# Kernel optimization log

Hardware: AMD Instinct MI355X
Metric: run time of the kernel (lower is better)

Reference implementation:

```python
import jax, jax.numpy as jnp
import numpy as np

SEQ_LEN = 4096
D_MODEL = 1024
OUT_DIM = 1024
KERNEL = 256
STRIDE = 16
NUM_HEADS = 16


def _p(key, *shape):
    return jax.random.normal(key, shape, dtype=jnp.float32) * 0.02


def setup_inputs() -> dict:
    key = jax.random.key(0)
    ks = jax.random.split(key, 12)
    return {
        "path": jax.random.normal(ks[0], (SEQ_LEN, D_MODEL), dtype=jnp.float32),
        # sliding_module (nn.MultiheadAttention, embed_dim=D_MODEL)
        "w_in1": _p(ks[1], 3 * D_MODEL, D_MODEL),
        "b_in1": jnp.zeros((3 * D_MODEL,), jnp.float32),
        "w_out1": _p(ks[2], D_MODEL, D_MODEL),
        "b_out1": jnp.zeros((D_MODEL,), jnp.float32),
        # linear_module
        "w_lin": _p(ks[3], OUT_DIM, D_MODEL),
        "b_lin": jnp.zeros((OUT_DIM,), jnp.float32),
        # accum_module (embed_dim=OUT_DIM)
        "w_in2": _p(ks[4], 3 * OUT_DIM, OUT_DIM),
        "b_in2": jnp.zeros((3 * OUT_DIM,), jnp.float32),
        "w_out2": _p(ks[5], OUT_DIM, OUT_DIM),
        "b_out2": jnp.zeros((OUT_DIM,), jnp.float32),
    }


def _mha(q, k, v, w_in, b_in, w_out, b_out, num_heads):
    """torch nn.MultiheadAttention math (dropout=0). q,k,v: [..., L, E]."""
    E = q.shape[-1]
    Dh = E // num_heads
    wq, wk, wv = jnp.split(w_in, 3, axis=0)
    bq, bk, bv = jnp.split(b_in, 3)
    def heads(t):
        return t.reshape(t.shape[:-1] + (num_heads, Dh))
    qh = heads(q @ wq.T + bq)
    kh = heads(k @ wk.T + bk)
    vh = heads(v @ wv.T + bv)
    scale = 1.0 / np.sqrt(Dh).astype(np.float32)
    att = jax.nn.softmax(jnp.einsum("...qhd,...khd->...hqk", qh, kh) * scale, axis=-1)
    out = jnp.einsum("...hqk,...khd->...qhd", att, vh)
    out = out.reshape(out.shape[:-2] + (E,))
    return out @ w_out.T + b_out


def reference(path, w_in1, b_in1, w_out1, b_out1, w_lin, b_lin,
              w_in2, b_in2, w_out2, b_out2):
    seq_len = path.shape[-2]
    slices_num = (seq_len - KERNEL) // STRIDE
    # overlapping windows: [slices_num, KERNEL, D_MODEL]
    idx = jnp.arange(slices_num)[:, None] * STRIDE + jnp.arange(KERNEL)[None, :]
    x = path[idx]
    # batched self-attention over windows
    x = _mha(x, x, x, w_in1, b_in1, w_out1, b_out1, NUM_HEADS)
    x = jax.nn.relu(x @ w_lin.T + b_lin)  # [slices_num, KERNEL, OUT_DIM]
    # sequential recurrent attention accumulation
    def step(cum_att, xi):
        new = _mha(xi, cum_att, cum_att, w_in2, b_in2, w_out2, b_out2, NUM_HEADS)
        return new, None
    cum_att, _ = jax.lax.scan(step, x[0], x[1:])
    return cum_att  # [KERNEL, OUT_DIM]
```

## Files before the change

kernel.cpp:

```cpp
#include <hip/hip_runtime.h>
#include <math.h>

#define D_MODEL 1024
#define N_WIN   240
#define TOK     256
#define NH      16
#define DH      64
#define CHUNK   8
#define NCHUNK  30
#define WIN     ((size_t)TOK * D_MODEL)

typedef unsigned short ushort_t;
typedef unsigned long long ull_t;
typedef __attribute__((ext_vector_type(8))) short short8;
typedef __attribute__((ext_vector_type(4))) float floatx4;

__device__ __forceinline__ ushort_t f2bf(float f) {
    unsigned u = __float_as_uint(f);
    unsigned lsb = (u >> 16) & 1u;
    u += 0x7fffu + lsb;
    return (ushort_t)(u >> 16);
}

__device__ __forceinline__ void st2_wt(ushort_t* p, ushort_t v) {
    unsigned vv = v;
    asm volatile("global_store_short %0, %1, off sc1"
                 :: "v"(p), "v"(vv) : "memory");
}
__device__ __forceinline__ void rel_drain() {
    asm volatile("s_waitcnt vmcnt(0)" ::: "memory");
}

#define GLDS(g, l) __builtin_amdgcn_global_load_lds( \
    (const __attribute__((address_space(1))) unsigned int*)(g), \
    (__attribute__((address_space(3))) unsigned int*)(l), 16, 0, 0)

__device__ __forceinline__ void grid_bar(unsigned* base, int g, unsigned s)
{
    rel_drain();
    __syncthreads();
    if (threadIdx.x == 0) {
        unsigned old = __hip_atomic_fetch_add(base + g * 32, 1u,
                __ATOMIC_RELAXED, __HIP_MEMORY_SCOPE_AGENT);
        if (old == 8u * s - 1u) {
            unsigned r = __hip_atomic_fetch_add(base + 256, 1u,
                    __ATOMIC_RELAXED, __HIP_MEMORY_SCOPE_AGENT);
            if (r == 8u * s - 1u)
                __hip_atomic_store(base + 288, s, __ATOMIC_RELAXED,
                                   __HIP_MEMORY_SCOPE_AGENT);
        }
        while (__hip_atomic_load(base + 288, __ATOMIC_RELAXED,
                                 __HIP_MEMORY_SCOPE_AGENT) < s)
            __builtin_amdgcn_s_sleep(1);
    }
    __syncthreads();
}

__device__ __forceinline__ void help_bar(unsigned* base, int g, unsigned s)
{
    rel_drain();
    __syncthreads();
    if (threadIdx.x == 0) {
        unsigned old = __hip_atomic_fetch_add(base + 1024 + g * 32, 1u,
                __ATOMIC_RELAXED, __HIP_MEMORY_SCOPE_AGENT);
        if (old == 8u * s - 1u) {
            unsigned r = __hip_atomic_fetch_add(base + 1800, 1u,
                    __ATOMIC_RELAXED, __HIP_MEMORY_SCOPE_AGENT);
            if (r == 24u * s - 1u)
                __hip_atomic_store(base + 1832, s, __ATOMIC_RELAXED,
                                   __HIP_MEMORY_SCOPE_AGENT);
        }
        while (__hip_atomic_load(base + 1832, __ATOMIC_RELAXED,
                                 __HIP_MEMORY_SCOPE_AGENT) < s)
            __builtin_amdgcn_s_sleep(1);
    }
    __syncthreads();
}

__global__ __launch_bounds__(256) void cast_bf_k(
    const float* __restrict__ s, ushort_t* __restrict__ d, int n)
{
    int i = (blockIdx.x * 256 + threadIdx.x) * 4;
    if (i >= n) return;
    float4 v = *(const float4*)(s + i);
    ushort4 o;
    o.x = f2bf(v.x); o.y = f2bf(v.y); o.z = f2bf(v.z); o.w = f2bf(v.w);
    *(ushort4*)(d + i) = o;
}

// ... 3 lines not shown
    __shared__ ushort_t t[64][65];
    const int bx = blockIdx.x * 64, by = blockIdx.y * 64;
    const int c = threadIdx.x & 63, r0 = threadIdx.x >> 6;
#pragma unroll
    for (int k = 0; k < 16; ++k) {
        int r = r0 + k * 4;
        t[r][c] = src[(size_t)(by + r) * 1024 + bx + c];
    }
    __syncthreads();
#pragma unroll
    for (int k = 0; k < 16; ++k) {
        int r = r0 + k * 4;
        dst[(size_t)(bx + r) * 1024 + by + c] = t[c][r];
    }
}

__global__ __launch_bounds__(256) void bc_k(
    const float* __restrict__ w_in2, const float* __restrict__ b_in2,
    const float* __restrict__ b_out2, float* __restrict__ bc)
{
    int n = blockIdx.x * 256 + threadIdx.x;
    const float* row = w_in2 + (size_t)(1024 + n) * 1024;
    float s = b_in2[1024 + n];
    for (int j = 0; j < 1024; j += 4) {
        float4 w = *(const float4*)(row + j);
        float4 b = *(const float4*)(b_out2 + j);
        s += w.x * b.x + w.y * b.y + w.z * b.z + w.w * b.w;
    }
    bc[n] = s;
}

template<bool GATHER, bool WT>
__device__ __forceinline__ void gemm_core(
    ushort_t* As, ushort_t* Bs,
    const ushort_t* __restrict__ A, int lda, int w0,
    const ushort_t* __restrict__ W, const float* __restrict__ bias,
    ushort_t* __restrict__ Cb, float* __restrict__ Cf, int ldc,
    int K, int m0, int n0, int co, int relu)
{
    const int tid = threadIdx.x;
    const int wave = tid >> 6, lane = tid & 63;
    const int wm = wave & 1, wn = wave >> 1;

    int r0 = m0 + (tid >> 2), r1 = r0 + 64;
    if (GATHER) {
        r0 = (w0 + (r0 >> 8)) * 16 + (r0 & 255);
        r1 = (w0 + (r1 >> 8)) * 16 + (r1 & 255);
    }
    const int kcol = (tid & 3) * 8;
    const ushort_t* gA0 = A + (size_t)r0 * lda + kcol;
    const ushort_t* gA1 = A + (size_t)r1 * lda + kcol;
    const ushort_t* pW  = W + (size_t)n0 * K;
    const ushort_t* gB0 = pW + (size_t)(tid >> 2) * K + kcol;
    const ushort_t* gB1 = gB0 + (size_t)64 * K;
    ushort_t* lA = As + wave * 512;
    ushort_t* lB = Bs + wave * 512;

    floatx4 acc[4][4];
#pragma unroll
    for (int i = 0; i < 4; ++i)
#pragma unroll
        for (int j = 0; j < 4; ++j) acc[i][j] = (floatx4){0.f, 0.f, 0.f, 0.f};

    const int fr = lane & 15, fk = (lane >> 4) * 8;
    const int arow = (wm * 64 + fr) * 32 + fk;
    const int brow = (wn * 64 + fr) * 32 + fk;

    for (int k0 = 0; k0 < K; k0 += 32) {
        GLDS(gA0 + k0, lA);
        GLDS(gA1 + k0, lA + 2048);
        GLDS(gB0 + k0, lB);
        GLDS(gB1 + k0, lB + 2048);
        __syncthreads();
// ... 13 lines not shown

    const int crq = (lane >> 4) * 4;
    const int ccol = lane & 15;
#pragma unroll
    for (int mi = 0; mi < 4; ++mi) {
#pragma unroll
        for (int ni = 0; ni < 4; ++ni) {
            int lc = wn * 64 + ni * 16 + ccol;
            float bz = bias[n0 + lc];
#pragma unroll
            for (int rg = 0; rg < 4; ++rg) {
                int row = m0 + wm * 64 + mi * 16 + crq + rg;
                float v = acc[mi][ni][rg] + bz;
                if (relu) v = fmaxf(v, 0.f);
                size_t off = (size_t)row * ldc + co + lc;
                if (Cb) {
                    if (WT) st2_wt(Cb + off, f2bf(v));
                    else    Cb[off] = f2bf(v);
                }
                if (Cf) Cf[off] = v;
            }
        }
    }
}

__global__ __launch_bounds__(256) void gemm_bf_k(
    const ushort_t* __restrict__ A, int lda,
    const ushort_t* __restrict__ W, const float* __restrict__ bias,
    ushort_t* __restrict__ Cb, float* __restrict__ Cf, int ldc,
    int K, int relu)
{
    __shared__ ushort_t As[128 * 32];
    __shared__ ushort_t Bs[128 * 32];
    gemm_core<false, false>(As, Bs, A, lda, 0, W, bias, Cb, Cf, ldc, K,
                            blockIdx.y * 128, blockIdx.x * 128, blockIdx.x * 128, relu);
}

__global__ __launch_bounds__(256) void gemm_qkv_k(
    const ushort_t* __restrict__ path_bf, const ushort_t* __restrict__ W,
    const float* __restrict__ bias, ushort_t* __restrict__ Cb, int w0)
{
    __shared__ ushort_t As[128 * 32];
    __shared__ ushort_t Bs[128 * 32];
    gemm_core<true, false>(As, Bs, path_bf, 1024, w0, W, bias, Cb, nullptr, 3072, 1024,
                           blockIdx.y * 128, blockIdx.x * 128, blockIdx.x * 128, 0);
}

#define PLD 260
#define VLD 132

struct AttnShared {
    ushort_t P[64 * PLD];
    ushort_t VT[64 * VLD];
    float    l[64];
};

__device__ void attn_body(AttnShared& sh,
    const ushort_t* __restrict__ qkv, ushort_t* __restrict__ ao,
    int rs, int h, int b)
{
    const ushort_t* base = qkv + (size_t)b * TOK * 3072;
    const ushort_t* Q = base;
    const ushort_t* K = base + 1024;
    const ushort_t* V = base + 2048;
    ushort_t* O = ao + (size_t)b * TOK * 1024;
    const int ldq = 3072, ldkv = 3072, ldo = 1024;
    const int tid = threadIdx.x;
    const int wave = tid >> 6, lane = tid & 63;
    const int fr = lane & 15, q = lane >> 4, fk = q * 8;
    const ushort_t* Qh = Q + (size_t)(rs * 64) * ldq + h * 64;
    const ushort_t* Kh = K + h * 64;
    const ushort_t* Vh = V + h * 64;
    const int m0 = wave * 16;

    floatx4 s[16];
#pragma unroll
    for (int nt = 0; nt < 16; ++nt) s[nt] = (floatx4){0.f, 0.f, 0.f, 0.f};
#pragma unroll
    for (int kc = 0; kc < 64; kc += 32) {
        short8 a = *(const short8*)(Qh + (size_t)(m0 + fr) * ldq + kc + fk);
#pragma unroll
        for (int nt = 0; nt < 16; ++nt) {
            short8 b2 = *(const short8*)(Kh + (size_t)(nt * 16 + fr) * ldkv + kc + fk);
            s[nt] = __builtin_amdgcn_mfma_f32_16x16x32_bf16(a, b2, s[nt], 0, 0, 0);
        }
    }

    float rmax[4] = {-INFINITY, -INFINITY, -INFINITY, -INFINITY};
#pragma unroll
    for (int nt = 0; nt < 16; ++nt)
#pragma unroll
        for (int rg = 0; rg < 4; ++rg) rmax[rg] = fmaxf(rmax[rg], s[nt][rg]);
#pragma unroll
    for (int d = 1; d < 16; d <<= 1)
#pragma unroll
        for (int rg = 0; rg < 4; ++rg)
            rmax[rg] = fmaxf(rmax[rg], __shfl_xor(rmax[rg], d));

    float rsum[4] = {0.f, 0.f, 0.f, 0.f};
#pragma unroll
// ... 39 lines not shown
            }
        }
        __syncthreads();
#pragma unroll
        for (int ks = 0; ks < 4; ++ks) {
            short8 a = *(const short8*)&sh.P[(m0 + fr) * PLD + half * 128 + ks * 32 + fk];
#pragma unroll
            for (int nt2 = 0; nt2 < 4; ++nt2) {
                short8 b2 = *(const short8*)&sh.VT[(nt2 * 16 + fr) * VLD + ks * 32 + fk];
                o[nt2] = __builtin_amdgcn_mfma_f32_16x16x32_bf16(a, b2, o[nt2], 0, 0, 0);
            }
        }
        __syncthreads();
    }

    float linv[4];
#pragma unroll
    for (int rg = 0; rg < 4; ++rg) linv[rg] = 1.f / sh.l[m0 + q * 4 + rg];
#pragma unroll
    for (int nt2 = 0; nt2 < 4; ++nt2)
#pragma unroll
        for (int rg = 0; rg < 4; ++rg) {
            int row = rs * 64 + m0 + q * 4 + rg;
            st2_wt(O + (size_t)row * ldo + h * 64 + nt2 * 16 + fr,
                   f2bf(o[nt2][rg] * linv[rg]));
        }
    __syncthreads();
}

__global__ __launch_bounds__(256) void attn_mfma_k(
    const ushort_t* __restrict__ qkv, ushort_t* __restrict__ ao)
{
    __shared__ AttnShared sh;
    attn_body(sh, qkv, ao, blockIdx.x, blockIdx.y, blockIdx.z);
}

#define KLD 72
#define TLD 264

struct ScanSmem {
    union {
        struct { ushort_t Ab[2][16384]; ushort_t Wb[2][8192]; } st;
        struct { ushort_t Kl[256 * KLD]; ushort_t Vt[64 * TLD];
                 ushort_t P[64 * TLD]; } at;
    };
};

__device__ __forceinline__ void stage_kv(
    const ushort_t* __restrict__ Asrc, const ushort_t* __restrict__ Wsel,
    int h, int k0, ushort_t* __restrict__ Ad, ushort_t* __restrict__ Wd,
    int wave, int lane)
{
#pragma unroll
    for (int t = 0; t < 8; ++t) {
        int j = wave * 512 + t * 64 + lane;
        int row = j >> 3;
        int blk = (j & 7) ^ (row & 7);
        GLDS(Asrc + (size_t)row * 1024 + k0 + blk * 8,
             Ad + wave * 4096 + t * 512);
    }
#pragma unroll
    for (int t = 0; t < 4; ++t) {
        int j = wave * 256 + t * 64 + lane;
        int r = j >> 3;
        int blk = (j & 7) ^ (r & 7);
        int n = ((r >> 6) << 10) + h * 64 + (r & 63);
        GLDS(Wsel + (size_t)n * 1024 + k0 + blk * 8,
             Wd + wave * 2048 + t * 512);
    }
}

__device__ void scan_body(
    ScanSmem& sm, int h, int rs, int g,
    const ushort_t* __restrict__ Qchunk, int i0, int w0, int nsteps,
    const ushort_t* __restrict__ x0, ushort_t* __restrict__ AOb,
    const ushort_t* __restrict__ Wkv, const float* __restrict__ bkv,
    const ushort_t* __restrict__ Wc, const float* __restrict__ bc,
    unsigned* __restrict__ bar, unsigned s0)
{
    const int tid = threadIdx.x;
    const int wave = tid >> 6, lane = tid & 63;
    const int fr = lane & 15, q = lane >> 4, fk = q * 8;

    float bkK[4], bkV[4], bcK[4], bcV[4];
#pragma unroll
    for (int nt = 0; nt < 4; ++nt) {
        bkK[nt] = bkv[h * 64 + nt * 16 + fr];
        bkV[nt] = bkv[1024 + h * 64 + nt * 16 + fr];
        bcK[nt] = bc[h * 64 + nt * 16 + fr];
        bcV[nt] = bc[1024 + h * 64 + nt * 16 + fr];
    }

    ushort_t* Kl = sm.at.Kl;
    ushort_t* Vt = sm.at.Vt;
    ushort_t* P  = sm.at.P;

    unsigned s = s0;
    for (int t0 = 0; t0 < nsteps; ++t0, ++s) {
        const int i = i0 + t0;
        const ushort_t* Asrc;
        const ushort_t* Wsel;
        if (i == 1) { Asrc = x0; Wsel = Wkv; }
        else {
            Asrc = AOb + (size_t)((i - 1) & 7) * WIN;
            Wsel = Wc;
        }

        const int m0g = rs * 64 + wave * 16;
        const ushort_t* Qrow = Qchunk + (size_t)(i - w0) * WIN
            + (size_t)(m0g + fr) * 1024 + h * 64;
        short8 qf0 = *(const short8*)(Qrow);
        short8 qf1 = *(const short8*)(Qrow + 32);

        floatx4 acc[4][8];
#pragma unroll
        for (int mt = 0; mt < 4; ++mt)
#pragma unroll
            for (int nt = 0; nt < 8; ++nt)
                acc[mt][nt] = (floatx4){0.f, 0.f, 0.f, 0.f};

        stage_kv(Asrc, Wsel, h, 0, sm.st.Ab[0], sm.st.Wb[0], wave, lane);
#pragma unroll 1
        for (int t = 0; t < 16; ++t) {
            const int cur = t & 1;
            if (t < 15) {
                stage_kv(Asrc, Wsel, h, (t + 1) * 64,
                         sm.st.Ab[cur ^ 1], sm.st.Wb[cur ^ 1], wave, lane);
                asm volatile("s_waitcnt vmcnt(12)" ::: "memory");
            } else {
                asm volatile("s_waitcnt vmcnt(0)" ::: "memory");
            }
            __builtin_amdgcn_s_barrier();
            const ushort_t* Ac = sm.st.Ab[cur];
            const ushort_t* Wc_ = sm.st.Wb[cur];
#pragma unroll
            for (int kh = 0; kh < 2; ++kh) {
                const int pb = (((kh << 2) + q) ^ (fr & 7)) * 8;
                short8 a[4];
#pragma unroll
                for (int mt = 0; mt < 4; ++mt)
                    a[mt] = *(const short8*)
                        &Ac[(wave * 64 + mt * 16 + fr) * 64 + pb];
#pragma unroll
                for (int nt = 0; nt < 8; ++nt) {
                    const int r = ((nt >> 2) << 6) + ((nt & 3) << 4) + fr;
                    short8 b = *(const short8*)&Wc_[r * 64 + pb];
#pragma unroll
                    for (int mt = 0; mt < 4; ++mt)
                        acc[mt][nt] = __builtin_amdgcn_mfma_f32_16x16x32_bf16(
                            a[mt], b, acc[mt][nt], 0, 0, 0);
                }
            }
            asm volatile("s_waitcnt lgkmcnt(0)" ::: "memory");
            __builtin_amdgcn_sched_barrier(0);
            __builtin_amdgcn_s_barrier();
        }

#pragma unroll
        for (int mt = 0; mt < 4; ++mt) {
            const int kb = wave * 64 + mt * 16;
#pragma unroll
            for (int nt = 0; nt < 4; ++nt) {
                float bzk = (i == 1) ? bkK[nt] : bcK[nt];
                float bzv = (i == 1) ? bkV[nt] : bcV[nt];
#pragma unroll
                for (int rg = 0; rg < 4; ++rg)
                    Kl[(kb + q * 4 + rg) * KLD + nt * 16 + fr] =
                        f2bf(acc[mt][nt][rg] + bzk);
                ushort4 pv;
                pv.x = f2bf(acc[mt][nt + 4][0] + bzv);
                pv.y = f2bf(acc[mt][nt + 4][1] + bzv);
                pv.z = f2bf(acc[mt][nt + 4][2] + bzv);
                pv.w = f2bf(acc[mt][nt + 4][3] + bzv);
                *(ushort4*)&Vt[(nt * 16 + fr) * TLD + kb + q * 4] = pv;
            }
        }
        __syncthreads();

        ushort_t* AOcur = AOb + (size_t)(i & 7) * WIN;
        {
            const int pl0 = wave * 16;
            floatx4 sc[16];
#pragma unroll
            for (int nt = 0; nt < 16; ++nt) sc[nt] = (floatx4){0.f, 0.f, 0.f, 0.f};
#pragma unroll
            for (int kc = 0; kc < 64; kc += 32) {
                short8 a = (kc == 0) ? qf0 : qf1;
#pragma unroll
                for (int nt = 0; nt < 16; ++nt) {
                    short8 b = *(const short8*)&Kl[(nt * 16 + fr) * KLD + kc + fk];
                    sc[nt] = __builtin_amdgcn_mfma_f32_16x16x32_bf16(
                        a, b, sc[nt], 0, 0, 0);
                }
            }
            float rmax[4] = {-INFINITY, -INFINITY, -INFINITY, -INFINITY};
#pragma unroll
            for (int nt = 0; nt < 16; ++nt)
#pragma unroll
                for (int rg = 0; rg < 4; ++rg) rmax[rg] = fmaxf(rmax[rg], sc[nt][rg]);
#pragma unroll
            for (int d = 1; d < 16; d <<= 1)
#pragma unroll
                for (int rg = 0; rg < 4; ++rg)
                    rmax[rg] = fmaxf(rmax[rg], __shfl_xor(rmax[rg], d));
            float rsum[4] = {0.f, 0.f, 0.f, 0.f};
#pragma unroll
            for (int nt = 0; nt < 16; ++nt) {
#pragma unroll
                for (int rg = 0; rg < 4; ++rg) {
                    float p = __expf((sc[nt][rg] - rmax[rg]) * 0.125f);
                    rsum[rg] += p;
                    P[(pl0 + q * 4 + rg) * TLD + nt * 16 + fr] = f2bf(p);
                }
            }
#pragma unroll
            for (int d = 1; d < 16; d <<= 1)
#pragma unroll
                for (int rg = 0; rg < 4; ++rg) rsum[rg] += __shfl_xor(rsum[rg], d);

            floatx4 o[4];
#pragma unroll
            for (int nt = 0; nt < 4; ++nt) o[nt] = (floatx4){0.f, 0.f, 0.f, 0.f};
#pragma unroll
            for (int kt = 0; kt < 8; ++kt) {
                short8 a = *(const short8*)&P[(pl0 + fr) * TLD + kt * 32 + fk];
#pragma unroll
                for (int nt = 0; nt < 4; ++nt) {
                    short8 b = *(const short8*)&Vt[(nt * 16 + fr) * TLD + kt * 32 + fk];
                    o[nt] = __builtin_amdgcn_mfma_f32_16x16x32_bf16(
                        a, b, o[nt], 0, 0, 0);
                }
            }
            float linv[4];
#pragma unroll
            for (int rg = 0; rg < 4; ++rg) linv[rg] = 1.f / rsum[rg];
#pragma unroll
            for (int nt = 0; nt < 4; ++nt)
#pragma unroll
                for (int rg = 0; rg < 4; ++rg) {
                    int row = m0g + q * 4 + rg;
                    st2_wt(AOcur + (size_t)row * 1024 + h * 64 + nt * 16 + fr,
                           f2bf(o[nt][rg] * linv[rg]));
                }
        }
        grid_bar(bar, g, s);
    }
}

struct GemmSmem { ushort_t As[128 * 32]; ushort_t Bs[128 * 32]; };
union FusedSmem { ScanSmem scan; GemmSmem gem; AttnShared att; };

__global__ __launch_bounds__(256, 1) void fused_k(
    const ushort_t* __restrict__ Qchunk, int i0, int w0, int nsteps,
    const ushort_t* __restrict__ x0, ushort_t* __restrict__ AOb,
    const ushort_t* __restrict__ Wkv, const float* __restrict__ bkv,
    const ushort_t* __restrict__ Wc, const float* __restrict__ bc,
    unsigned* __restrict__ bar, unsigned s0,
    int do_help, int w0n,
    const ushort_t* __restrict__ path_bf,
    const ushort_t* __restrict__ w_in1, const float* __restrict__ b_in1,
    ushort_t* __restrict__ qkv, ushort_t* __restrict__ ao,
    ushort_t* __restrict__ ybuf,
    const ushort_t* __restrict__ w_out1, const float* __restrict__ b_out1,
    const ushort_t* __restrict__ w_lin, const float* __restrict__ b_lin,
    ushort_t* __restrict__ Xc,
    const ushort_t* __restrict__ w_in2, const float* __restrict__ b_in2,
    ushort_t* __restrict__ Qnext, unsigned hs0)
{
    __shared__ FusedSmem sm;
    const int wg = blockIdx.x;
    const int x = wg & 7, y = wg >> 3;

    if (x < 2) {
        const int scanIdx = x * 32 + y;
        const int h  = (x << 3) | (y >> 2);
        const int rs = y & 3;
        const int g  = scanIdx & 7;
        scan_body(sm.scan, h, rs, g,
                  Qchunk, i0, w0, nsteps, x0, AOb, Wkv, bkv, Wc, bc, bar, s0);
        return;
    }
    if (!do_help) return;

    const int hw = (x - 2) * 32 + y;
    const int hg = hw >> 3;

    for (int t = hw; t < 384; t += 192) {
        int bx = t % 24, by = t / 24;
        gemm_core<true, true>(sm.gem.As, sm.gem.Bs, path_bf, 1024, w0n,
                              w_in1, b_in1, qkv, nullptr, 3072, 1024,
                              by * 128, bx * 128, bx * 128, 0);
    }
    help_bar(bar, hg, hs0);

    for (int t = hw; t < 512; t += 192) {
        int rs = t & 3, h = (t >> 2) & 15, b = t >> 6;
        attn_body(sm.att, qkv, ao, rs, h, b);
    }
    help_bar(bar, hg, hs0 + 1);

    for (int t = hw; t < 128; t += 192) {
        int bx = t & 7, by = t >> 3;
        gemm_core<false, true>(sm.gem.As, sm.gem.Bs, ao, 1024, 0,
                               w_out1, b_out1, ybuf, nullptr, 1024, 1024,
                               by * 128, bx * 128, bx * 128, 0);
    }
    help_bar(bar, hg, hs0 + 2);

    for (int t = hw; t < 128; t += 192) {
        int bx = t & 7, by = t >> 3;
        gemm_core<false, true>(sm.gem.As, sm.gem.Bs, ybuf, 1024, 0,
                               w_lin, b_lin, Xc, nullptr, 1024, 1024,
                               by * 128, bx * 128, bx * 128, 1);
    }
    help_bar(bar, hg, hs0 + 3);

    for (int t = hw; t < 128; t += 192) {
        int bx = t & 7, by = t >> 3;
        gemm_core<false, true>(sm.gem.As, sm.gem.Bs, Xc, 1024, 0,
                               w_in2, b_in2, Qnext, nullptr, 1024, 1024,
                               by * 128, bx * 128, bx * 128, 0);
    }
}

extern "C" void kernel_launch(void* const* d_in, const int* in_sizes, int n_in,
                              void* d_out, int out_size, void* d_ws, size_t ws_size,
                              hipStream_t stream)
{
    const float* path   = (const float*)d_in[0];
    const float* w_in1  = (const float*)d_in[1];
    const float* b_in1  = (const float*)d_in[2];
    const float* w_out1 = (const float*)d_in[3];
    const float* b_out1 = (const float*)d_in[4];
    const float* w_lin  = (const float*)d_in[5];
    const float* b_lin  = (const float*)d_in[6];
    const float* w_in2  = (const float*)d_in[7];
    const float* b_in2  = (const float*)d_in[8];
    const float* w_out2 = (const float*)d_in[9];
    const float* b_out2 = (const float*)d_in[10];
    float* out = (float*)d_out;

    unsigned* bar = (unsigned*)d_ws;
    float* bc      = (float*)d_ws + 2048;
    float* zerosf  = bc + 2048;
    ushort_t* ws = (ushort_t*)d_ws + 16384;
    ushort_t* path_bf  = ws;
    ushort_t* w_in1_bf = path_bf  + (size_t)4096 * 1024;
    ushort_t* w_out1_bf= w_in1_bf + (size_t)3072 * 1024;
    ushort_t* w_lin_bf = w_out1_bf+ (size_t)1024 * 1024;
    ushort_t* w_in2_bf = w_lin_bf + (size_t)1024 * 1024;
    ushort_t* w_out2_bf= w_in2_bf + (size_t)3072 * 1024;
    ushort_t* WoT_bf   = w_out2_bf+ (size_t)1024 * 1024;
    ushort_t* Wc_bf    = WoT_bf   + (size_t)1024 * 1024;
    ushort_t* qkv_bf   = Wc_bf    + (size_t)2048 * 1024;
    ushort_t* ao_bf    = qkv_bf   + (size_t)2048 * 3072;
    ushort_t* ybuf_bf  = ao_bf    + (size_t)2048 * 1024;
    ushort_t* Xbuf     = ybuf_bf  + (size_t)2048 * 1024;
    ushort_t* Qb0      = Xbuf     + (size_t)2048 * 1024;
    ushort_t* Qb1      = Qb0      + (size_t)2048 * 1024;
    ushort_t* AOb      = Qb1      + (size_t)2048 * 1024;
    ushort_t* x0buf    = AOb + 8 * WIN;
    ushort_t* dummy    = x0buf + WIN;
    ushort_t* Qb[2] = {Qb0, Qb1};

    hipMemsetAsync(bar, 0, 8192, stream);
    hipMemsetAsync(zerosf, 0, 1024 * sizeof(float), stream);

    cast_bf_k<<<4096, 256, 0, stream>>>(path,  path_bf,  4096 * 1024);
    cast_bf_k<<<3072, 256, 0, stream>>>(w_in1, w_in1_bf, 3072 * 1024);
    cast_bf_k<<<1024, 256, 0, stream>>>(w_out1, w_out1_bf, 1024 * 1024);
    cast_bf_k<<<1024, 256, 0, stream>>>(w_lin, w_lin_bf, 1024 * 1024);
    cast_bf_k<<<3072, 256, 0, stream>>>(w_in2, w_in2_bf, 3072 * 1024);
    cast_bf_k<<<1024, 256, 0, stream>>>(w_out2, w_out2_bf, 1024 * 1024);

    transpose_k<<<dim3(16, 16), 256, 0, stream>>>(w_out2_bf, WoT_bf);
    bc_k<<<8, 256, 0, stream>>>(w_in2, b_in2, b_out2, bc);
    gemm_bf_k<<<dim3(8, 16), 256, 0, stream>>>(
        w_in2_bf + (size_t)1024 * 1024, 1024, WoT_bf, zerosf,
        Wc_bf, nullptr, 1024, 1024, 0);

    gemm_qkv_k<<<dim3(24, 16), 256, 0, stream>>>(
        path_bf, w_in1_bf, b_in1, qkv_bf, 0);
    attn_mfma_k<<<dim3(4, NH, CHUNK), 256, 0, stream>>>(qkv_bf, ao_bf);
    gemm_bf_k<<<dim3(8, 16), 256, 0, stream>>>(
        ao_bf, 1024, w_out1_bf, b_out1, ybuf_bf, nullptr, 1024, 1024, 0);
    gemm_bf_k<<<dim3(8, 16), 256, 0, stream>>>(
        ybuf_bf, 1024, w_lin_bf, b_lin, Xbuf, nullptr, 1024, 1024, 1);
    gemm_bf_k<<<dim3(8, 16), 256, 0, stream>>>(
        Xbuf, 1024, w_in2_bf, b_in2, Qb[0], nullptr, 1024, 1024, 0);
    hipMemcpyAsync(x0buf, Xbuf, WIN * sizeof(ushort_t),
                   hipMemcpyDeviceToDevice, stream);

    unsigned sbase = 1;
    for (int c = 0; c < NCHUNK; ++c) {
        int w0 = c * CHUNK;
        int i0 = (c == 0) ? 1 : w0;
        int nsteps = (c == 0) ? CHUNK - 1 : CHUNK;
        int do_help = (c + 1 < NCHUNK) ? 1 : 0;
        int w0n = (c + 1) * CHUNK;
        unsigned hs0 = (unsigned)(c * 4 + 1);
        const ushort_t* Qcur = Qb[c & 1];
        ushort_t* Qnext = Qb[(c + 1) & 1];
        const ushort_t* x0P = x0buf;
        ushort_t* AObP = AOb;
        const ushort_t* WkvP = w_in2_bf + (size_t)1024 * 1024;
        const float* bkvP = b_in2 + 1024;
        const ushort_t* WcP = Wc_bf;
        const float* bcP = bc;
        unsigned* barP = bar;
        unsigned sb = sbase;
        const ushort_t* pathP = path_bf;
        const ushort_t* win1P = w_in1_bf;
        const float* bin1P = b_in1;
        ushort_t* qkvP = qkv_bf;
        ushort_t* aoP = ao_bf;
        ushort_t* ybufP = ybuf_bf;
        const ushort_t* wout1P = w_out1_bf;
        const float* bout1P = b_out1;
        const ushort_t* wlinP = w_lin_bf;
        const float* blinP = b_lin;
        ushort_t* XP = Xbuf;
        const ushort_t* win2P = w_in2_bf;
        const float* bin2P = b_in2;
        void* args[] = {&Qcur, &i0, &w0, &nsteps, &x0P, &AObP,
                        &WkvP, &bkvP, &WcP, &bcP, &barP, &sb,
                        &do_help, &w0n, &pathP, &win1P, &bin1P,
                        &qkvP, &aoP, &ybufP, &wout1P, &bout1P,
                        &wlinP, &blinP, &XP, &win2P, &bin2P, &Qnext, &hs0};
        hipLaunchCooperativeKernel((void*)fused_k, dim3(256), dim3(256),
                                   args, 0, stream);
        sbase += (unsigned)nsteps;
    }

    gemm_bf_k<<<dim3(8, 2), 256, 0, stream>>>(
        AOb + (size_t)((N_WIN - 1) & 7) * WIN, 1024, w_out2_bf, b_out2,
        dummy, out, 1024, 1024, 0);
}
```

Measured before the change: 7.043 ms.

## Split per-head K/V projection across row-slice blocks and exchange via global buffer

Each of the four row-slice blocks per head now computes K/V projections for only its 64 keys, instead of recomputing the full 256-key projection redundantly. Results go to a global KV exchange buffer with write-through stores, a new per-head barrier synchronises the four blocks, and each block then reloads the full K and V into shared memory. This cuts the redundant GEMM work and staging traffic four-fold, at the cost of an extra global round trip, a per-head spin barrier each step, and a changed shared-memory padding.

```diff
diff --git a/kernel.cpp b/kernel.cpp
--- a/kernel.cpp
+++ b/kernel.cpp
@@ -51,6 +51,20 @@
         }
         while (__hip_atomic_load(base + 288, __ATOMIC_RELAXED,
                                  __HIP_MEMORY_SCOPE_AGENT) < s)
+            __builtin_amdgcn_s_sleep(1);
+    }
+    __syncthreads();
+}
+
+__device__ __forceinline__ void head_bar(unsigned* base, int h, unsigned s)
+{
+    rel_drain();
+    __syncthreads();
+    if (threadIdx.x == 0) {
+        __hip_atomic_fetch_add(base + 384 + h * 32, 1u,
+                __ATOMIC_RELAXED, __HIP_MEMORY_SCOPE_AGENT);
+        while (__hip_atomic_load(base + 384 + h * 32, __ATOMIC_RELAXED,
+                                 __HIP_MEMORY_SCOPE_AGENT) < 4u * s)
             __builtin_amdgcn_s_sleep(1);
     }
     __syncthreads();
@@ -352,29 +366,29 @@
     attn_body(sh, qkv, ao, blockIdx.x, blockIdx.y, blockIdx.z);
 }
 
-#define KLD 72
+#define KLD 76
 #define TLD 264
 
 struct ScanSmem {
     union {
-        struct { ushort_t Ab[2][16384]; ushort_t Wb[2][8192]; } st;
+        struct { ushort_t Ab[2][4096]; ushort_t Wb[2][8192]; } st;
         struct { ushort_t Kl[256 * KLD]; ushort_t Vt[64 * TLD];
                  ushort_t P[64 * TLD]; } at;
     };
 };
 
 __device__ __forceinline__ void stage_kv(
-    const ushort_t* __restrict__ Asrc, const ushort_t* __restrict__ Wsel,
+    const ushort_t* __restrict__ A64, const ushort_t* __restrict__ Wsel,
     int h, int k0, ushort_t* __restrict__ Ad, ushort_t* __restrict__ Wd,
     int wave, int lane)
 {
 #pragma unroll
-    for (int t = 0; t < 8; ++t) {
-        int j = wave * 512 + t * 64 + lane;
+    for (int t = 0; t < 2; ++t) {
+        int j = wave * 128 + t * 64 + lane;
         int row = j >> 3;
         int blk = (j & 7) ^ (row & 7);
-        GLDS(Asrc + (size_t)row * 1024 + k0 + blk * 8,
-             Ad + wave * 4096 + t * 512);
+        GLDS(A64 + (size_t)row * 1024 + k0 + blk * 8,
+             Ad + wave * 1024 + t * 512);
     }
 #pragma unroll
     for (int t = 0; t < 4; ++t) {
@@ -391,6 +405,7 @@
     ScanSmem& sm, int h, int rs, int g,
     const ushort_t* __restrict__ Qchunk, int i0, int w0, int nsteps,
     const ushort_t* __restrict__ x0, ushort_t* __restrict__ AOb,
+    ushort_t* __restrict__ KVx,
     const ushort_t* __restrict__ Wkv, const float* __restrict__ bkv,
     const ushort_t* __restrict__ Wc, const float* __restrict__ bc,
     unsigned* __restrict__ bar, unsigned s0)
@@ -399,13 +414,12 @@
     const int wave = tid >> 6, lane = tid & 63;
     const int fr = lane & 15, q = lane >> 4, fk = q * 8;
 
-    float bkK[4], bkV[4], bcK[4], bcV[4];
-#pragma unroll
-    for (int nt = 0; nt < 4; ++nt) {
-        bkK[nt] = bkv[h * 64 + nt * 16 + fr];
-        bkV[nt] = bkv[1024 + h * 64 + nt * 16 + fr];
-        bcK[nt] = bc[h * 64 + nt * 16 + fr];
-        bcV[nt] = bc[1024 + h * 64 + nt * 16 + fr];
+    const int dbofs = (wave < 2 ? 0 : 1024) + h * 64 + (wave & 1) * 32;
+    float bK1[2], bC1[2];
+#pragma unroll
+    for (int nt = 0; nt < 2; ++nt) {
+        bK1[nt] = bkv[dbofs + nt * 16 + fr];
+        bC1[nt] = bc[dbofs + nt * 16 + fr];
     }
 
     ushort_t* Kl = sm.at.Kl;
@@ -422,6 +436,8 @@
             Asrc = AOb + (size_t)((i - 1) & 7) * WIN;
             Wsel = Wc;
         }
+        const ushort_t* A64 = Asrc + (size_t)rs * 64 * 1024;
+        ushort_t* KVs = KVx + (size_t)(i & 7) * (NH * 32768) + h * 32768;
 
         const int m0g = rs * 64 + wave * 16;
         const ushort_t* Qrow = Qchunk + (size_t)(i - w0) * WIN
@@ -429,21 +445,21 @@
         short8 qf0 = *(const short8*)(Qrow);
         short8 qf1 = *(const short8*)(Qrow + 32);
 
-        floatx4 acc[4][8];
+        floatx4 acc[4][2];
 #pragma unroll
         for (int mt = 0; mt < 4; ++mt)
 #pragma unroll
-            for (int nt = 0; nt < 8; ++nt)
+            for (int nt = 0; nt < 2; ++nt)
                 acc[mt][nt] = (floatx4){0.f, 0.f, 0.f, 0.f};
 
-        stage_kv(Asrc, Wsel, h, 0, sm.st.Ab[0], sm.st.Wb[0], wave, lane);
+        stage_kv(A64, Wsel, h, 0, sm.st.Ab[0], sm.st.Wb[0], wave, lane);
 #pragma unroll 1
         for (int t = 0; t < 16; ++t) {
             const int cur = t & 1;
             if (t < 15) {
-                stage_kv(Asrc, Wsel, h, (t + 1) * 64,
+                stage_kv(A64, Wsel, h, (t + 1) * 64,
                          sm.st.Ab[cur ^ 1], sm.st.Wb[cur ^ 1], wave, lane);
-                asm volatile("s_waitcnt vmcnt(12)" ::: "memory");
+                asm volatile("s_waitcnt vmcnt(6)" ::: "memory");
             } else {
                 asm volatile("s_waitcnt vmcnt(0)" ::: "memory");
             }
@@ -456,12 +472,11 @@
                 short8 a[4];
 #pragma unroll
                 for (int mt = 0; mt < 4; ++mt)
-                    a[mt] = *(const short8*)
-                        &Ac[(wave * 64 + mt * 16 + fr) * 64 + pb];
-#pragma unroll
-                for (int nt = 0; nt < 8; ++nt) {
-                    const int r = ((nt >> 2) << 6) + ((nt & 3) << 4) + fr;
-                    short8 b = *(const short8*)&Wc_[r * 64 + pb];
+                    a[mt] = *(const short8*)&Ac[(mt * 16 + fr) * 64 + pb];
+#pragma unroll
+                for (int nt = 0; nt < 2; ++nt) {
+                    short8 b = *(const short8*)
+                        &Wc_[(wave * 32 + nt * 16 + fr) * 64 + pb];
 #pragma unroll
                     for (int mt = 0; mt < 4; ++mt)
                         acc[mt][nt] = __builtin_amdgcn_mfma_f32_16x16x32_bf16(
@@ -473,23 +488,51 @@
             __builtin_amdgcn_s_barrier();
         }
 
-#pragma unroll
-        for (int mt = 0; mt < 4; ++mt) {
-            const int kb = wave * 64 + mt * 16;
-#pragma unroll
-            for (int nt = 0; nt < 4; ++nt) {
-                float bzk = (i == 1) ? bkK[nt] : bcK[nt];
-                float bzv = (i == 1) ? bkV[nt] : bcV[nt];
-#pragma unroll
-                for (int rg = 0; rg < 4; ++rg)
-                    Kl[(kb + q * 4 + rg) * KLD + nt * 16 + fr] =
-                        f2bf(acc[mt][nt][rg] + bzk);
-                ushort4 pv;
-                pv.x = f2bf(acc[mt][nt + 4][0] + bzv);
-                pv.y = f2bf(acc[mt][nt + 4][1] + bzv);
-                pv.z = f2bf(acc[mt][nt + 4][2] + bzv);
-                pv.w = f2bf(acc[mt][nt + 4][3] + bzv);
-                *(ushort4*)&Vt[(nt * 16 + fr) * TLD + kb + q * 4] = pv;
+        {
+            ushort_t* Kx = KVs;
+            ushort_t* Vx = KVs + 16384;
+#pragma unroll
+            for (int mt = 0; mt < 4; ++mt) {
+#pragma unroll
+                for (int nt = 0; nt < 2; ++nt) {
+                    const float bz = (i == 1) ? bK1[nt] : bC1[nt];
+                    const int d = (wave & 1) * 32 + nt * 16 + fr;
+#pragma unroll
+                    for (int rg = 0; rg < 4; ++rg) {
+                        const int key = rs * 64 + mt * 16 + q * 4 + rg;
+                        const float v = acc[mt][nt][rg] + bz;
+                        if (wave < 2) st2_wt(Kx + key * 64 + d, f2bf(v));
+                        else          st2_wt(Vx + d * 256 + key, f2bf(v));
+                    }
+                }
+            }
+        }
+        head_bar(bar, h, s);
+
+        {
+            const ushort_t* Kx = KVs;
+            const ushort_t* Vx = KVs + 16384;
+            uint4 kb4[8], vb4[8];
+            const ushort_t* kr = Kx + tid * 64;
+            const int vd = tid >> 2, vq = tid & 3;
+            const ushort_t* vr = Vx + vd * 256 + vq * 64;
+#pragma unroll
+            for (int s8 = 0; s8 < 8; ++s8)
+                kb4[s8] = *(const uint4*)(kr + s8 * 8);
+#pragma unroll
+            for (int s8 = 0; s8 < 8; ++s8)
+                vb4[s8] = *(const uint4*)(vr + s8 * 8);
+            const int kp = (tid >> 4) & 3;
+#pragma unroll
+            for (int s8 = 0; s8 < 8; ++s8) {
+                int ks = (s8 + kp) & 7;
+                *(uint4*)&Kl[tid * KLD + ks * 8] = kb4[ks];
+            }
+            const int vp = vq << 1;
+#pragma unroll
+            for (int s8 = 0; s8 < 8; ++s8) {
+                int vs = (s8 + vp) & 7;
+                *(uint4*)&Vt[vd * TLD + vq * 64 + vs * 8] = vb4[vs];
             }
         }
         __syncthreads();
@@ -570,6 +613,7 @@
 __global__ __launch_bounds__(256, 1) void fused_k(
     const ushort_t* __restrict__ Qchunk, int i0, int w0, int nsteps,
     const ushort_t* __restrict__ x0, ushort_t* __restrict__ AOb,
+    ushort_t* __restrict__ KVx,
     const ushort_t* __restrict__ Wkv, const float* __restrict__ bkv,
     const ushort_t* __restrict__ Wc, const float* __restrict__ bc,
     unsigned* __restrict__ bar, unsigned s0,
@@ -594,7 +638,8 @@
         const int rs = y & 3;
         const int g  = scanIdx & 7;
         scan_body(sm.scan, h, rs, g,
-                  Qchunk, i0, w0, nsteps, x0, AOb, Wkv, bkv, Wc, bc, bar, s0);
+                  Qchunk, i0, w0, nsteps, x0, AOb, KVx,
+                  Wkv, bkv, Wc, bc, bar, s0);
         return;
     }
     if (!do_help) return;
@@ -678,6 +723,7 @@
     ushort_t* AOb      = Qb1      + (size_t)2048 * 1024;
     ushort_t* x0buf    = AOb + 8 * WIN;
     ushort_t* dummy    = x0buf + WIN;
+    ushort_t* KVx      = dummy + WIN;
     ushort_t* Qb[2] = {Qb0, Qb1};
 
     hipMemsetAsync(bar, 0, 8192, stream);
@@ -720,6 +766,7 @@
         ushort_t* Qnext = Qb[(c + 1) & 1];
         const ushort_t* x0P = x0buf;
         ushort_t* AObP = AOb;
+        ushort_t* KVxP = KVx;
         const ushort_t* WkvP = w_in2_bf + (size_t)1024 * 1024;
         const float* bkvP = b_in2 + 1024;
         const ushort_t* WcP = Wc_bf;
@@ -739,7 +786,7 @@
         ushort_t* XP = Xbuf;
         const ushort_t* win2P = w_in2_bf;
         const float* bin2P = b_in2;
-        void* args[] = {&Qcur, &i0, &w0, &nsteps, &x0P, &AObP,
+        void* args[] = {&Qcur, &i0, &w0, &nsteps, &x0P, &AObP, &KVxP,
                         &WkvP, &bkvP, &WcP, &bcP, &barP, &sb,
                         &do_help, &w0n, &pathP, &win1P, &bin1P,
                         &qkvP, &aoP, &ybufP, &wout1P, &bout1P,
```

Result: no change. 6.972 ms (-1.0%).

## Use 512-thread blocks: one scan block per head, paired helper tiles

Applied to the files above, without the earlier changes.

Doubles the fused cooperative kernel's block size to 512 threads. Each sequential-scan head is now handled by a single block, with waves split into K and V sections and two query passes, so only 16 scan blocks synchronize instead of 64. The KV GEMM gets triple-buffered weight staging, and the next step's weights and Q fragments are prefetched while waiting at the barrier. Helper blocks process two GEMM or attention tiles per block, one per 256-thread half, and write out-of-range tiles to a dummy buffer. The cost is fewer scan blocks, each doing more serial work per step, plus higher register and shared-memory pressure from the larger blocks.

```diff
diff --git a/kernel.cpp b/kernel.cpp
--- a/kernel.cpp
+++ b/kernel.cpp
@@ -34,27 +34,6 @@
 #define GLDS(g, l) __builtin_amdgcn_global_load_lds( \
     (const __attribute__((address_space(1))) unsigned int*)(g), \
     (__attribute__((address_space(3))) unsigned int*)(l), 16, 0, 0)
-
-__device__ __forceinline__ void grid_bar(unsigned* base, int g, unsigned s)
-{
-    rel_drain();
-    __syncthreads();
-    if (threadIdx.x == 0) {
-        unsigned old = __hip_atomic_fetch_add(base + g * 32, 1u,
-                __ATOMIC_RELAXED, __HIP_MEMORY_SCOPE_AGENT);
-        if (old == 8u * s - 1u) {
-            unsigned r = __hip_atomic_fetch_add(base + 256, 1u,
-                    __ATOMIC_RELAXED, __HIP_MEMORY_SCOPE_AGENT);
-            if (r == 8u * s - 1u)
-                __hip_atomic_store(base + 288, s, __ATOMIC_RELAXED,
-                                   __HIP_MEMORY_SCOPE_AGENT);
-        }
-        while (__hip_atomic_load(base + 288, __ATOMIC_RELAXED,
-                                 __HIP_MEMORY_SCOPE_AGENT) < s)
-            __builtin_amdgcn_s_sleep(1);
-    }
-    __syncthreads();
-}
 
 __device__ __forceinline__ void help_bar(unsigned* base, int g, unsigned s)
 {
@@ -124,13 +103,12 @@
 
 template<bool GATHER, bool WT>
 __device__ __forceinline__ void gemm_core(
-    ushort_t* As, ushort_t* Bs,
+    ushort_t* As, ushort_t* Bs, int tid,
     const ushort_t* __restrict__ A, int lda, int w0,
     const ushort_t* __restrict__ W, const float* __restrict__ bias,
     ushort_t* __restrict__ Cb, float* __restrict__ Cf, int ldc,
     int K, int m0, int n0, int co, int relu)
 {
-    const int tid = threadIdx.x;
     const int wave = tid >> 6, lane = tid & 63;
     const int wm = wave & 1, wn = wave >> 1;
 
@@ -210,7 +188,7 @@
 {
     __shared__ ushort_t As[128 * 32];
     __shared__ ushort_t Bs[128 * 32];
-    gemm_core<false, false>(As, Bs, A, lda, 0, W, bias, Cb, Cf, ldc, K,
+    gemm_core<false, false>(As, Bs, threadIdx.x, A, lda, 0, W, bias, Cb, Cf, ldc, K,
                             blockIdx.y * 128, blockIdx.x * 128, blockIdx.x * 128, relu);
 }
 
@@ -220,7 +198,8 @@
 {
     __shared__ ushort_t As[128 * 32];
     __shared__ ushort_t Bs[128 * 32];
-    gemm_core<true, false>(As, Bs, path_bf, 1024, w0, W, bias, Cb, nullptr, 3072, 1024,
+    gemm_core<true, false>(As, Bs, threadIdx.x, path_bf, 1024, w0, W, bias, Cb,
+                           nullptr, 3072, 1024,
                            blockIdx.y * 128, blockIdx.x * 128, blockIdx.x * 128, 0);
 }
 
@@ -233,7 +212,7 @@
     float    l[64];
 };
 
-__device__ void attn_body(AttnShared& sh,
+__device__ void attn_body(AttnShared& sh, int tid,
     const ushort_t* __restrict__ qkv, ushort_t* __restrict__ ao,
     int rs, int h, int b)
 {
@@ -243,7 +222,6 @@
     const ushort_t* V = base + 2048;
     ushort_t* O = ao + (size_t)b * TOK * 1024;
     const int ldq = 3072, ldkv = 3072, ldo = 1024;
-    const int tid = threadIdx.x;
     const int wave = tid >> 6, lane = tid & 63;
     const int fr = lane & 15, q = lane >> 4, fk = q * 8;
     const ushort_t* Qh = Q + (size_t)(rs * 64) * ldq + h * 64;
@@ -349,46 +327,51 @@
     const ushort_t* __restrict__ qkv, ushort_t* __restrict__ ao)
 {
     __shared__ AttnShared sh;
-    attn_body(sh, qkv, ao, blockIdx.x, blockIdx.y, blockIdx.z);
-}
-
-#define KLD 72
+    attn_body(sh, threadIdx.x, qkv, ao, blockIdx.x, blockIdx.y, blockIdx.z);
+}
+
+#define KLD 76
 #define TLD 264
 
 struct ScanSmem {
     union {
-        struct { ushort_t Ab[2][16384]; ushort_t Wb[2][8192]; } st;
+        struct { ushort_t Ab[2][16384]; ushort_t Wb[3][8192]; } st;
         struct { ushort_t Kl[256 * KLD]; ushort_t Vt[64 * TLD];
-                 ushort_t P[64 * TLD]; } at;
+                 ushort_t P[128 * TLD]; } at;
     };
 };
 
-__device__ __forceinline__ void stage_kv(
-    const ushort_t* __restrict__ Asrc, const ushort_t* __restrict__ Wsel,
-    int h, int k0, ushort_t* __restrict__ Ad, ushort_t* __restrict__ Wd,
+__device__ __forceinline__ void stage_A(
+    const ushort_t* __restrict__ Asrc, int k0, ushort_t* __restrict__ Ad,
     int wave, int lane)
 {
 #pragma unroll
-    for (int t = 0; t < 8; ++t) {
-        int j = wave * 512 + t * 64 + lane;
+    for (int t = 0; t < 4; ++t) {
+        int j = wave * 256 + t * 64 + lane;
         int row = j >> 3;
         int blk = (j & 7) ^ (row & 7);
         GLDS(Asrc + (size_t)row * 1024 + k0 + blk * 8,
-             Ad + wave * 4096 + t * 512);
-    }
-#pragma unroll
-    for (int t = 0; t < 4; ++t) {
-        int j = wave * 256 + t * 64 + lane;
+             Ad + wave * 2048 + t * 512);
+    }
+}
+
+__device__ __forceinline__ void stage_W(
+    const ushort_t* __restrict__ Wsel, int h, int k0,
+    ushort_t* __restrict__ Wd, int wave, int lane)
+{
+#pragma unroll
+    for (int t = 0; t < 2; ++t) {
+        int j = wave * 128 + t * 64 + lane;
         int r = j >> 3;
         int blk = (j & 7) ^ (r & 7);
         int n = ((r >> 6) << 10) + h * 64 + (r & 63);
         GLDS(Wsel + (size_t)n * 1024 + k0 + blk * 8,
-             Wd + wave * 2048 + t * 512);
+             Wd + wave * 1024 + t * 512);
     }
 }
 
 __device__ void scan_body(
-    ScanSmem& sm, int h, int rs, int g,
+    ScanSmem& sm, int h,
     const ushort_t* __restrict__ Qchunk, int i0, int w0, int nsteps,
     const ushort_t* __restrict__ x0, ushort_t* __restrict__ AOb,
     const ushort_t* __restrict__ Wkv, const float* __restrict__ bkv,
@@ -398,70 +381,76 @@
     const int tid = threadIdx.x;
     const int wave = tid >> 6, lane = tid & 63;
     const int fr = lane & 15, q = lane >> 4, fk = q * 8;
-
-    float bkK[4], bkV[4], bcK[4], bcV[4];
+    const int kw = wave & 3, sec = wave >> 2;
+    const int g = h & 7;
+
+    const int dbofs = sec * 1024 + h * 64;
+    float bK[4], bC[4];
 #pragma unroll
     for (int nt = 0; nt < 4; ++nt) {
-        bkK[nt] = bkv[h * 64 + nt * 16 + fr];
-        bkV[nt] = bkv[1024 + h * 64 + nt * 16 + fr];
-        bcK[nt] = bc[h * 64 + nt * 16 + fr];
-        bcV[nt] = bc[1024 + h * 64 + nt * 16 + fr];
+        bK[nt] = bkv[dbofs + nt * 16 + fr];
+        bC[nt] = bc[dbofs + nt * 16 + fr];
     }
 
     ushort_t* Kl = sm.at.Kl;
     ushort_t* Vt = sm.at.Vt;
     ushort_t* P  = sm.at.P;
 
+    short8 qf00, qf01, qf10, qf11;
+    {
+        const int i = i0;
+        const ushort_t* Wsel0 = (i == 1) ? Wkv : Wc;
+        stage_W(Wsel0, h, 0,  sm.st.Wb[0], wave, lane);
+        stage_W(Wsel0, h, 64, sm.st.Wb[1], wave, lane);
+        const ushort_t* Qr = Qchunk + (size_t)(i - w0) * WIN
+            + (size_t)(wave * 16 + fr) * 1024 + h * 64;
+        qf00 = *(const short8*)(Qr);
+        qf01 = *(const short8*)(Qr + 32);
+        qf10 = *(const short8*)(Qr + (size_t)128 * 1024);
+        qf11 = *(const short8*)(Qr + (size_t)128 * 1024 + 32);
+        const ushort_t* Asrc0 = (i == 1) ? x0
+            : AOb + (size_t)((i - 1) & 7) * WIN;
+        stage_A(Asrc0, 0, sm.st.Ab[0], wave, lane);
+    }
+
     unsigned s = s0;
     for (int t0 = 0; t0 < nsteps; ++t0, ++s) {
         const int i = i0 + t0;
-        const ushort_t* Asrc;
-        const ushort_t* Wsel;
-        if (i == 1) { Asrc = x0; Wsel = Wkv; }
-        else {
-            Asrc = AOb + (size_t)((i - 1) & 7) * WIN;
-            Wsel = Wc;
-        }
-
-        const int m0g = rs * 64 + wave * 16;
-        const ushort_t* Qrow = Qchunk + (size_t)(i - w0) * WIN
-            + (size_t)(m0g + fr) * 1024 + h * 64;
-        short8 qf0 = *(const short8*)(Qrow);
-        short8 qf1 = *(const short8*)(Qrow + 32);
-
-        floatx4 acc[4][8];
+        const ushort_t* Asrc = (i == 1) ? x0
+            : AOb + (size_t)((i - 1) & 7) * WIN;
+        const ushort_t* Wsel = (i == 1) ? Wkv : Wc;
+
+        floatx4 acc[4][4];
 #pragma unroll
         for (int mt = 0; mt < 4; ++mt)
 #pragma unroll
-            for (int nt = 0; nt < 8; ++nt)
+            for (int nt = 0; nt < 4; ++nt)
                 acc[mt][nt] = (floatx4){0.f, 0.f, 0.f, 0.f};
 
-        stage_kv(Asrc, Wsel, h, 0, sm.st.Ab[0], sm.st.Wb[0], wave, lane);
 #pragma unroll 1
         for (int t = 0; t < 16; ++t) {
-            const int cur = t & 1;
-            if (t < 15) {
-                stage_kv(Asrc, Wsel, h, (t + 1) * 64,
-                         sm.st.Ab[cur ^ 1], sm.st.Wb[cur ^ 1], wave, lane);
-                asm volatile("s_waitcnt vmcnt(12)" ::: "memory");
-            } else {
+            if (t < 15)
+                stage_A(Asrc, (t + 1) * 64, sm.st.Ab[(t + 1) & 1], wave, lane);
+            if (t < 14)
+                stage_W(Wsel, h, (t + 2) * 64, sm.st.Wb[(t + 2) % 3], wave, lane);
+            if (t == 15)
                 asm volatile("s_waitcnt vmcnt(0)" ::: "memory");
-            }
+            else
+                asm volatile("s_waitcnt vmcnt(6)" ::: "memory");
             __builtin_amdgcn_s_barrier();
-            const ushort_t* Ac = sm.st.Ab[cur];
-            const ushort_t* Wc_ = sm.st.Wb[cur];
+            const ushort_t* Ac  = sm.st.Ab[t & 1];
+            const ushort_t* Wc_ = sm.st.Wb[t % 3];
 #pragma unroll
             for (int kh = 0; kh < 2; ++kh) {
                 const int pb = (((kh << 2) + q) ^ (fr & 7)) * 8;
                 short8 a[4];
 #pragma unroll
                 for (int mt = 0; mt < 4; ++mt)
-                    a[mt] = *(const short8*)
-                        &Ac[(wave * 64 + mt * 16 + fr) * 64 + pb];
-#pragma unroll
-                for (int nt = 0; nt < 8; ++nt) {
-                    const int r = ((nt >> 2) << 6) + ((nt & 3) << 4) + fr;
-                    short8 b = *(const short8*)&Wc_[r * 64 + pb];
+                    a[mt] = *(const short8*)&Ac[(kw * 64 + mt * 16 + fr) * 64 + pb];
+#pragma unroll
+                for (int nt = 0; nt < 4; ++nt) {
+                    short8 b = *(const short8*)
+                        &Wc_[(sec * 64 + nt * 16 + fr) * 64 + pb];
 #pragma unroll
                     for (int mt = 0; mt < 4; ++mt)
                         acc[mt][nt] = __builtin_amdgcn_mfma_f32_16x16x32_bf16(
@@ -475,34 +464,37 @@
 
 #pragma unroll
         for (int mt = 0; mt < 4; ++mt) {
-            const int kb = wave * 64 + mt * 16;
 #pragma unroll
             for (int nt = 0; nt < 4; ++nt) {
-                float bzk = (i == 1) ? bkK[nt] : bcK[nt];
-                float bzv = (i == 1) ? bkV[nt] : bcV[nt];
-#pragma unroll
-                for (int rg = 0; rg < 4; ++rg)
-                    Kl[(kb + q * 4 + rg) * KLD + nt * 16 + fr] =
-                        f2bf(acc[mt][nt][rg] + bzk);
-                ushort4 pv;
-                pv.x = f2bf(acc[mt][nt + 4][0] + bzv);
-                pv.y = f2bf(acc[mt][nt + 4][1] + bzv);
-                pv.z = f2bf(acc[mt][nt + 4][2] + bzv);
-                pv.w = f2bf(acc[mt][nt + 4][3] + bzv);
-                *(ushort4*)&Vt[(nt * 16 + fr) * TLD + kb + q * 4] = pv;
+                const float bz = (i == 1) ? bK[nt] : bC[nt];
+                if (sec == 0) {
+#pragma unroll
+                    for (int rg = 0; rg < 4; ++rg)
+                        Kl[(kw * 64 + mt * 16 + q * 4 + rg) * KLD + nt * 16 + fr]
+                            = f2bf(acc[mt][nt][rg] + bz);
+                } else {
+                    ushort4 pv;
+                    pv.x = f2bf(acc[mt][nt][0] + bz);
+                    pv.y = f2bf(acc[mt][nt][1] + bz);
+                    pv.z = f2bf(acc[mt][nt][2] + bz);
+                    pv.w = f2bf(acc[mt][nt][3] + bz);
+                    *(ushort4*)&Vt[(nt * 16 + fr) * TLD
+                                   + kw * 64 + mt * 16 + q * 4] = pv;
+                }
             }
         }
         __syncthreads();
 
         ushort_t* AOcur = AOb + (size_t)(i & 7) * WIN;
-        {
+        auto attn_pass = [&](int p, short8 a0, short8 a1) {
+            const int m0g = p * 128 + wave * 16;
             const int pl0 = wave * 16;
             floatx4 sc[16];
 #pragma unroll
             for (int nt = 0; nt < 16; ++nt) sc[nt] = (floatx4){0.f, 0.f, 0.f, 0.f};
 #pragma unroll
             for (int kc = 0; kc < 64; kc += 32) {
-                short8 a = (kc == 0) ? qf0 : qf1;
+                short8 a = (kc == 0) ? a0 : a1;
 #pragma unroll
                 for (int nt = 0; nt < 16; ++nt) {
                     short8 b = *(const short8*)&Kl[(nt * 16 + fr) * KLD + kc + fk];
@@ -525,9 +517,9 @@
             for (int nt = 0; nt < 16; ++nt) {
 #pragma unroll
                 for (int rg = 0; rg < 4; ++rg) {
-                    float p = __expf((sc[nt][rg] - rmax[rg]) * 0.125f);
-                    rsum[rg] += p;
-                    P[(pl0 + q * 4 + rg) * TLD + nt * 16 + fr] = f2bf(p);
+                    float pp = __expf((sc[nt][rg] - rmax[rg]) * 0.125f);
+                    rsum[rg] += pp;
+                    P[(pl0 + q * 4 + rg) * TLD + nt * 16 + fr] = f2bf(pp);
                 }
             }
 #pragma unroll
@@ -559,15 +551,49 @@
                     st2_wt(AOcur + (size_t)row * 1024 + h * 64 + nt * 16 + fr,
                            f2bf(o[nt][rg] * linv[rg]));
                 }
-        }
-        grid_bar(bar, g, s);
+        };
+        attn_pass(0, qf00, qf01);
+        attn_pass(1, qf10, qf11);
+
+        rel_drain();
+        __syncthreads();
+        if (tid == 0) {
+            unsigned old = __hip_atomic_fetch_add(bar + g * 32, 1u,
+                    __ATOMIC_RELAXED, __HIP_MEMORY_SCOPE_AGENT);
+            if (old == 2u * s - 1u) {
+                unsigned r = __hip_atomic_fetch_add(bar + 256, 1u,
+                        __ATOMIC_RELAXED, __HIP_MEMORY_SCOPE_AGENT);
+                if (r == 8u * s - 1u)
+                    __hip_atomic_store(bar + 288, s, __ATOMIC_RELAXED,
+                                       __HIP_MEMORY_SCOPE_AGENT);
+            }
+        }
+        const bool more = (t0 + 1 < nsteps);
+        if (more) {
+            stage_W(Wc, h, 0,  sm.st.Wb[0], wave, lane);
+            stage_W(Wc, h, 64, sm.st.Wb[1], wave, lane);
+            const ushort_t* Qn = Qchunk + (size_t)(i + 1 - w0) * WIN
+                + (size_t)(wave * 16 + fr) * 1024 + h * 64;
+            qf00 = *(const short8*)(Qn);
+            qf01 = *(const short8*)(Qn + 32);
+            qf10 = *(const short8*)(Qn + (size_t)128 * 1024);
+            qf11 = *(const short8*)(Qn + (size_t)128 * 1024 + 32);
+        }
+        if (tid == 0) {
+            while (__hip_atomic_load(bar + 288, __ATOMIC_RELAXED,
+                                     __HIP_MEMORY_SCOPE_AGENT) < s)
+                __builtin_amdgcn_s_sleep(1);
+        }
+        __syncthreads();
+        if (more)
+            stage_A(AOb + (size_t)(i & 7) * WIN, 0, sm.st.Ab[0], wave, lane);
     }
 }
 
 struct GemmSmem { ushort_t As[128 * 32]; ushort_t Bs[128 * 32]; };
-union FusedSmem { ScanSmem scan; GemmSmem gem; AttnShared att; };
-
-__global__ __launch_bounds__(256, 1) void fused_k(
+union FusedSmem { ScanSmem scan; GemmSmem gem[2]; AttnShared att[2]; };
+
+__global__ __launch_bounds__(512, 2) void fused_k(
     const ushort_t* __restrict__ Qchunk, int i0, int w0, int nsteps,
     const ushort_t* __restrict__ x0, ushort_t* __restrict__ AOb,
     const ushort_t* __restrict__ Wkv, const float* __restrict__ bkv,
@@ -582,60 +608,70 @@
     const ushort_t* __restrict__ w_lin, const float* __restrict__ b_lin,
     ushort_t* __restrict__ Xc,
     const ushort_t* __restrict__ w_in2, const float* __restrict__ b_in2,
-    ushort_t* __restrict__ Qnext, unsigned hs0)
+    ushort_t* __restrict__ Qnext, unsigned hs0,
+    ushort_t* __restrict__ dummy_g)
 {
     __shared__ FusedSmem sm;
     const int wg = blockIdx.x;
     const int x = wg & 7, y = wg >> 3;
 
     if (x < 2) {
-        const int scanIdx = x * 32 + y;
-        const int h  = (x << 3) | (y >> 2);
-        const int rs = y & 3;
-        const int g  = scanIdx & 7;
-        scan_body(sm.scan, h, rs, g,
+        if (y >= 8) return;
+        scan_body(sm.scan, x * 8 + y,
                   Qchunk, i0, w0, nsteps, x0, AOb, Wkv, bkv, Wc, bc, bar, s0);
         return;
     }
     if (!do_help) return;
 
+    const int tid2 = (int)threadIdx.x & 255;
+    const int half = (int)threadIdx.x >> 8;
     const int hw = (x - 2) * 32 + y;
     const int hg = hw >> 3;
-
-    for (int t = hw; t < 384; t += 192) {
-        int bx = t % 24, by = t / 24;
-        gemm_core<true, true>(sm.gem.As, sm.gem.Bs, path_bf, 1024, w0n,
-                              w_in1, b_in1, qkv, nullptr, 3072, 1024,
-                              by * 128, bx * 128, bx * 128, 0);
+    const int slot = hw * 2 + half;
+
+    {
+        int t = slot, bx = t % 24, by = t / 24;
+        gemm_core<true, true>(sm.gem[half].As, sm.gem[half].Bs, tid2,
+                              path_bf, 1024, w0n, w_in1, b_in1, qkv, nullptr,
+                              3072, 1024, by * 128, bx * 128, bx * 128, 0);
     }
     help_bar(bar, hg, hs0);
 
-    for (int t = hw; t < 512; t += 192) {
-        int rs = t & 3, h = (t >> 2) & 15, b = t >> 6;
-        attn_body(sm.att, qkv, ao, rs, h, b);
+    for (int it = 0; it < 2; ++it) {
+        int t = slot + it * 384;
+        bool valid = (t < 512);
+        int tt = valid ? t : 0;
+        attn_body(sm.att[half], tid2, qkv, valid ? ao : dummy_g,
+                  tt & 3, (tt >> 2) & 15, tt >> 6);
     }
     help_bar(bar, hg, hs0 + 1);
 
-    for (int t = hw; t < 128; t += 192) {
-        int bx = t & 7, by = t >> 3;
-        gemm_core<false, true>(sm.gem.As, sm.gem.Bs, ao, 1024, 0,
-                               w_out1, b_out1, ybuf, nullptr, 1024, 1024,
+    {
+        bool valid = (slot < 128);
+        int t = valid ? slot : 0, bx = t & 7, by = t >> 3;
+        gemm_core<false, true>(sm.gem[half].As, sm.gem[half].Bs, tid2,
+                               ao, 1024, 0, w_out1, b_out1,
+                               valid ? ybuf : dummy_g, nullptr, 1024, 1024,
                                by * 128, bx * 128, bx * 128, 0);
     }
     help_bar(bar, hg, hs0 + 2);
 
-    for (int t = hw; t < 128; t += 192) {
-        int bx = t & 7, by = t >> 3;
-        gemm_core<false, true>(sm.gem.As, sm.gem.Bs, ybuf, 1024, 0,
-                               w_lin, b_lin, Xc, nullptr, 1024, 1024,
+    {
+        bool valid = (slot < 128);
+        int t = valid ? slot : 0, bx = t & 7, by = t >> 3;
+        gemm_core<false, true>(sm.gem[half].As, sm.gem[half].Bs, tid2,
+                               ybuf, 1024, 0, w_lin, b_lin,
+                               valid ? Xc : dummy_g, nullptr, 1024, 1024,
                                by * 128, bx * 128, bx * 128, 1);
     }
     help_bar(bar, hg, hs0 + 3);
 
-    for (int t = hw; t < 128; t += 192) {
-        int bx = t & 7, by = t >> 3;
-        gemm_core<false, true>(sm.gem.As, sm.gem.Bs, Xc, 1024, 0,
-                               w_in2, b_in2, Qnext, nullptr, 1024, 1024,
+    {
+        bool valid = (slot < 128);
+        int t = valid ? slot : 0, bx = t & 7, by = t >> 3;
+        gemm_core<false, true>(sm.gem[half].As, sm.gem[half].Bs, tid2,
+                               Xc, 1024, 0, w_in2, b_in2,
+                               valid ? Qnext : dummy_g, nullptr, 1024, 1024,
                                by * 128, bx * 128, bx * 128, 0);
     }
 }
@@ -705,8 +741,8 @@
         ybuf_bf, 1024, w_lin_bf, b_lin, Xbuf, nullptr, 1024, 1024, 1);
     gemm_bf_k<<<dim3(8, 16), 256, 0, stream>>>(
         Xbuf, 1024, w_in2_bf, b_in2, Qb[0], nullptr, 1024, 1024, 0);
-    hipMemcpyAsync(x0buf, Xbuf, WIN * sizeof(ushort_t),
-                   hipMemcpyDeviceToDevice, stream);
+    (void)hipMemcpyAsync(x0buf, Xbuf, WIN * sizeof(ushort_t),
+                         hipMemcpyDeviceToDevice, stream);
 
     unsigned sbase = 1;
     for (int c = 0; c < NCHUNK; ++c) {
@@ -739,12 +775,14 @@
         ushort_t* XP = Xbuf;
         const ushort_t* win2P = w_in2_bf;
         const float* bin2P = b_in2;
+        ushort_t* dummyP = dummy;
         void* args[] = {&Qcur, &i0, &w0, &nsteps, &x0P, &AObP,
                         &WkvP, &bkvP, &WcP, &bcP, &barP, &sb,
                         &do_help, &w0n, &pathP, &win1P, &bin1P,
                         &qkvP, &aoP, &ybufP, &wout1P, &bout1P,
-                        &wlinP, &blinP, &XP, &win2P, &bin2P, &Qnext, &hs0};
-        hipLaunchCooperativeKernel((void*)fused_k, dim3(256), dim3(256),
+                        &wlinP, &blinP, &XP, &win2P, &bin2P, &Qnext, &hs0,
+                        &dummyP};
+        hipLaunchCooperativeKernel((void*)fused_k, dim3(256), dim3(512),
                                    args, 0, stream);
         sbase += (unsigned)nsteps;
     }
```

Result: slower. 13.08 ms (+85.8%).
